# Optimization experiments

Measured on AMD Instinct MI355X. Metric: run time of the kernel, lower is better.

## Reference

```python
import jax, jax.numpy as jnp
import numpy as np

T_STEPS, N, STATE, HID, ACT, C = 32, 64, 64, 128, 32, 96


def setup_inputs() -> dict:
    key = jax.random.key(0)
    ks = jax.random.split(key, 16)
    s = 0.05
    inp = {
        'x': jax.random.normal(ks[0], (T_STEPS, N, STATE), jnp.float32),
        'a': jax.random.normal(ks[1], (T_STEPS, N, ACT), jnp.float32),
        # GRU layer 0 (input state_dim) and layer 1 (input hidden_dim)
        'wih0': jax.random.normal(ks[2], (3 * HID, STATE), jnp.float32) * s,
        'whh0': jax.random.normal(ks[3], (3 * HID, HID), jnp.float32) * s,
        'bih0': jax.random.normal(ks[4], (3 * HID,), jnp.float32) * s,
        'bhh0': jax.random.normal(ks[5], (3 * HID,), jnp.float32) * s,
        'wih1': jax.random.normal(ks[6], (3 * HID, HID), jnp.float32) * s,
        'whh1': jax.random.normal(ks[7], (3 * HID, HID), jnp.float32) * s,
        'bih1': jax.random.normal(ks[8], (3 * HID,), jnp.float32) * s,
        'bhh1': jax.random.normal(ks[9], (3 * HID,), jnp.float32) * s,
        'w1': jax.random.normal(ks[10], (HID, HID + ACT), jnp.float32) * s,
        'b1': jax.random.normal(ks[11], (HID,), jnp.float32) * s,
        'w2': jax.random.normal(ks[12], (1, 2 * HID), jnp.float32) * s,
        'b2': jax.random.normal(ks[13], (1,), jnp.float32) * s,
        'Tm': jax.random.normal(ks[14], (HID, HID, C), jnp.float32),  # init.normal(T,0,1)
    }
    return inp


def _gru_cell(x_t, h, wih, whh, bih, bhh):
    gi = x_t @ wih.T + bih            # (N, 3H)
    gh = h @ whh.T + bhh
    i_r, i_z, i_n = jnp.split(gi, 3, axis=-1)
    h_r, h_z, h_n = jnp.split(gh, 3, axis=-1)
    r = jax.nn.sigmoid(i_r + h_r)
    z = jax.nn.sigmoid(i_z + h_z)
    n = jnp.tanh(i_n + r * h_n)
    return (1.0 - z) * n + z * h


def reference(x, a, wih0, whh0, bih0, bhh0, wih1, whh1, bih1, bhh1, w1, b1, w2, b2, Tm):
    def step(h, x_t):
        h0 = _gru_cell(x_t, h[0], wih0, whh0, bih0, bhh0)
        h1 = _gru_cell(h0, h[1], wih1, whh1, bih1, bhh1)
        return jnp.stack([h0, h1]), h1

    h_init = jnp.zeros((2, N, HID), x.dtype)
    _, p = jax.lax.scan(step, h_init, x)              # (T, N, H)

    fc1 = jax.nn.relu(jnp.concatenate([p, a], -1) @ w1.T + b1)  # (T, N, H)

    Tflat = Tm.reshape(HID, HID * C)

    def batch_discrim(xt):  # xt: (N, H)
        M = (xt @ Tflat).reshape(N, HID, C)           # (N, B, C)
        # pairwise L1 over C: (N, N, B)
        norm = jnp.abs(M[:, None] - M[None, :]).sum(-1)
        o_b = (jnp.exp(-norm).sum(0) - 1.0) / (N - 1)  # (N, B)
        return jnp.concatenate([xt, o_b], 1)          # (N, 2H)

    fc2 = jax.lax.map(batch_discrim, fc1)             # (T, N, 2H)
    prob = jax.nn.sigmoid(fc2 @ w2.T + b2)            # (T, N, 1)
    return prob
```

## Files before the change

### kernel.cpp

```cpp
#include <hip/hip_runtime.h>
#include <hip/hip_fp16.h>
#include <cstdint>

#define T_STEPS 32
#define NB 64
#define STATE 64
#define HID 128
#define ACT 32
#define CDIM 96
#define G3 (3*HID)

typedef __attribute__((ext_vector_type(8))) short short8;
typedef __attribute__((ext_vector_type(4))) float f32x4;
typedef _Float16 h2v __attribute__((ext_vector_type(2)));

__device__ __forceinline__ unsigned short f2bf(float f){
  unsigned int u = __builtin_bit_cast(unsigned int, f);
  u = u + 0x7FFFu + ((u >> 16) & 1u);
  return (unsigned short)(u >> 16);
}
__device__ __forceinline__ float bf2f(unsigned short u){
  unsigned int v = ((unsigned int)u) << 16; return __builtin_bit_cast(float, v);
}
__device__ __forceinline__ unsigned int packh2(float f0, float f1){
  return (unsigned int)__half_as_ushort(__float2half_rn(f0)) |
         ((unsigned int)__half_as_ushort(__float2half_rn(f1)) << 16);
}
__device__ __forceinline__ float sigmoidf_(float x){ return 1.0f/(1.0f + __expf(-x)); }
__device__ __forceinline__ float tanhf_(float x){ float e = __expf(2.0f*x); return (e-1.0f)/(e+1.0f); }

__device__ __forceinline__ float dot2f(float acc, unsigned int a, unsigned int b){
  h2v av = __builtin_bit_cast(h2v, a);
  h2v bv = __builtin_bit_cast(h2v, b);
  return __builtin_amdgcn_fdot2(av, bv, acc, false);
}
__device__ __forceinline__ float l1d(float acc, unsigned int ua, unsigned int ub){
  __half2 a = __builtin_bit_cast(__half2, ua);
  __half2 b = __builtin_bit_cast(__half2, ub);
  __half2 d = __habs2(__hsub2(a, b));
  h2v dv = __builtin_bit_cast(h2v, d);
  h2v ones; ones[0] = (_Float16)1.0f; ones[1] = (_Float16)1.0f;
  return __builtin_amdgcn_fdot2(dv, ones, acc, false);
}
__device__ __forceinline__ float l1d4(float acc, uint4 a, uint4 b){
  acc = l1d(acc, a.x, b.x); acc = l1d(acc, a.y, b.y);
  acc = l1d(acc, a.z, b.z); acc = l1d(acc, a.w, b.w);
  return acc;
}

__global__ void k_prep(const float* __restrict__ Tm, unsigned short* __restrict__ tmh,
                       const float* __restrict__ whh0, const float* __restrict__ whh1,
                       const float* __restrict__ w1, const float* __restrict__ wih0,
                       const float* __restrict__ wih1, const float* __restrict__ x,
                       const float* __restrict__ a,
                       unsigned int* __restrict__ whh0p, unsigned int* __restrict__ whh1p,
                       unsigned short* __restrict__ w1f, unsigned short* __restrict__ wi0f,
                       unsigned short* __restrict__ wi1f, unsigned short* __restrict__ xaf,
                       unsigned short* __restrict__ h1af){
  __shared__ __align__(4) unsigned short lt[12800];
  int tid = threadIdx.x;
  int bx = blockIdx.x;
  if (bx < 128){
    int b = bx;
    unsigned int* l2 = (unsigned int*)lt;
    for (int e4 = tid; e4 < 3072; e4 += 256){
      int k = e4 / 24, c4 = (e4 - k*24)*4;
      const float4 v = *(const float4*)(Tm + k*(HID*CDIM) + b*CDIM + c4);
      int base = (k*100 + c4) >> 1;
      l2[base]   = (unsigned int)f2bf(v.x) | ((unsigned int)f2bf(v.y) << 16);
      l2[base+1] = (unsigned int)f2bf(v.z) | ((unsigned int)f2bf(v.w) << 16);
    }
    __syncthreads();
    unsigned int* tm2 = (unsigned int*)(tmh + b*(HID*CDIM));
    for (int e2 = tid; e2 < 6144; e2 += 256){
      int e = e2*2;
      int chunk = e / 768;
      int r1 = e - chunk*768;
      int c = r1 >> 3, h = r1 & 7;
      unsigned int lo = lt[(chunk*8 + h)*100 + c];
      unsigned int hi = lt[(chunk*8 + h + 1)*100 + c];
      tm2[e2] = lo | (hi << 16);
    }
  } else if (bx < 132){
    for (int e = (bx-128)*256 + tid; e < 24576; e += 1024){
      int k2 = e / 384, r = e - k2*384;
      whh0p[e] = packh2(whh0[r*128 + 2*k2], whh0[r*128 + 2*k2 + 1]);
      whh1p[e] = packh2(whh1[r*128 + 2*k2], whh1[r*128 + 2*k2 + 1]);
    }
  } else if (bx < 136){
    for (int e = (bx-132)*256 + tid; e < 20480; e += 1024){
      int kc = e >> 10, rem = e & 1023;
      int col = rem >> 3, j = rem & 7;
      w1f[e] = f2bf(w1[col*160 + kc*8 + j]);
    }
  } else if (bx < 140){
    for (int e = (bx-136)*256 + tid; e < 24576; e += 1024){
      int kc = e / 3072, rem = e - kc*3072;
      int col = rem >> 3, kl = rem & 7;
      wi0f[e] = f2bf(wih0[col*64 + kc*8 + kl]);
    }
  } else if (bx < 144){
    for (int e = (bx-140)*256 + tid; e < 49152; e += 1024){
      int kc = e / 3072, rem = e - kc*3072;
      int col = rem >> 3, kl = rem & 7;
      wi1f[e] = f2bf(wih1[col*128 + kc*8 + kl]);
    }
  } else if (bx < 156){
    for (int e = (bx-144)*256 + tid; e < 131072; e += 3072){
      int t = e >> 12, rem = e & 4095;
      int ntile = rem >> 10, rem2 = rem & 1023;
      int kc = rem2 >> 7, nl = (rem2 >> 3) & 15, kl = rem2 & 7;
      int n = ntile*16 + nl, k = kc*8 + kl;
      xaf[e] = f2bf(x[t*4096 + n*64 + k]);
    }
  } else {
    for (int e = (bx-156)*256 + tid; e < 65536; e += 3072){
      int t = e >> 11, rem = e & 2047;
      int n = rem >> 5, c = rem & 31;
      int pos = t*10240 + (n>>4)*2560 + (16 + (c>>3))*128 + (n&15)*8 + (c&7);
      h1af[pos] = f2bf(a[t*(NB*ACT) + n*ACT + c]);
    }
  }
}

template<int KK, int TSU>
__global__ __launch_bounds__(256) void k_gi(const unsigned short* __restrict__ af,
                                            const unsigned short* __restrict__ wf,
                                            const float* __restrict__ bias,
                                            float* __restrict__ gig){
  int t = blockIdx.x, by = blockIdx.y, tid = threadIdx.x;
  int wave = tid >> 6, lane = tid & 63, m = lane & 15, quad = lane >> 4;
  const uint4* A4 = (const uint4*)af;
  const uint4* B4 = (const uint4*)wf;
  uint4 av[KK];
  #pragma unroll
  for (int kk = 0; kk < KK; kk++) av[kk] = A4[t*TSU + wave*(TSU/4) + (kk*4+quad)*16 + m];
  f32x4 acc[6];
  #pragma unroll
  for (int i = 0; i < 6; i++) acc[i] = (f32x4)(0.0f);
  #pragma unroll
  for (int kk = 0; kk < KK; kk++){
    short8 a = __builtin_bit_cast(short8, av[kk]);
    #pragma unroll
    for (int ntl = 0; ntl < 6; ntl++){
      int nt = by*6 + ntl;
      uint4 bv = B4[(kk*4+quad)*384 + nt*16 + m];
      acc[ntl] = __builtin_amdgcn_mfma_f32_16x16x32_bf16(a, __builtin_bit_cast(short8, bv), acc[ntl], 0, 0, 0);
    }
  }
  #pragma unroll
  for (int ntl = 0; ntl < 6; ntl++){
    int col = (by*6+ntl)*16 + m;
    float bv = bias[col];
    #pragma unroll
    for (int rr = 0; rr < 4; rr++){
      int n = wave*16 + quad*4 + rr;
      gig[(t*NB + n)*G3 + col] = acc[ntl][rr] + bv;
    }
  }
}

template<int TS, int NS>
__global__ __launch_bounds__(768, 3) void k_rec(const unsigned int* __restrict__ whhp,
                                                const float* __restrict__ bhh,
                                                const float* __restrict__ gig,
                                                unsigned short* __restrict__ haf){
  __shared__ __align__(16) unsigned int hl[64];
  __shared__ float A0[G3];
  int n = blockIdx.x, tid = threadIdx.x;
  int r = tid >> 1, kh = tid & 1;
  unsigned int wh[32];
  #pragma unroll
  for (int i = 0; i < 32; i++) wh[i] = whhp[(kh*32 + i)*384 + r];
  float bh = (kh == 0) ? bhh[r] : 0.0f;
  if (tid < 64) hl[tid] = 0u;
  float g_r = 0.0f, g_z = 0.0f, g_n = 0.0f, hprev = 0.0f;
  if (tid < HID){
    const float* gp = gig + n*G3 + tid;
    g_r = gp[0]; g_z = gp[HID]; g_n = gp[2*HID];
  }
  __syncthreads();
  const uint4* h4 = (const uint4*)hl;
  for (int t = 0; t < T_STEPS; t++){
    float s0 = 0.0f, s1 = 0.0f, s2 = 0.0f, s3 = 0.0f;
    #pragma unroll
    for (int g = 0; g < 2; g++){
      uint4 hv[4];
      #pragma unroll
      for (int j = 0; j < 4; j++) hv[j] = h4[kh*8 + g*4 + j];
      s0 = dot2f(s0, wh[g*16 + 0], hv[0].x);  s0 = dot2f(s0, wh[g*16 + 1], hv[0].y);
      s0 = dot2f(s0, wh[g*16 + 2], hv[0].z);  s0 = dot2f(s0, wh[g*16 + 3], hv[0].w);
      s1 = dot2f(s1, wh[g*16 + 4], hv[1].x);  s1 = dot2f(s1, wh[g*16 + 5], hv[1].y);
      s1 = dot2f(s1, wh[g*16 + 6], hv[1].z);  s1 = dot2f(s1, wh[g*16 + 7], hv[1].w);
      s2 = dot2f(s2, wh[g*16 + 8], hv[2].x);  s2 = dot2f(s2, wh[g*16 + 9], hv[2].y);
      s2 = dot2f(s2, wh[g*16 +10], hv[2].z);  s2 = dot2f(s2, wh[g*16 +11], hv[2].w);
      s3 = dot2f(s3, wh[g*16 +12], hv[3].x);  s3 = dot2f(s3, wh[g*16 +13], hv[3].y);
      s3 = dot2f(s3, wh[g*16 +14], hv[3].z);  s3 = dot2f(s3, wh[g*16 +15], hv[3].w);
    }
    float gh = bh + ((s0 + s1) + (s2 + s3));
    gh += __shfl_xor(gh, 1);
    if (kh == 0) A0[r] = gh;
    __syncthreads();
    if (tid < HID){
      float cr = g_r, cz = g_z, cn = g_n;
      int tn2 = (t+1 < T_STEPS) ? t+1 : t;
      const float* gp = gig + (tn2*NB + n)*G3 + tid;
      g_r = gp[0]; g_z = gp[HID]; g_n = gp[2*HID];
      float rg = sigmoidf_(cr + A0[tid]);
      float z  = sigmoidf_(cz + A0[tid+HID]);
      float nn = tanhf_   (cn + rg*A0[tid+2*HID]);
      float hn = (1.0f - z)*nn + z*hprev;
      hprev = hn;
      ((__half*)hl)[tid] = __float2half_rn(hn);
      haf[t*TS + (n>>4)*NS + (tid>>3)*128 + (n&15)*8 + (tid&7)] = f2bf(hn);
    }
    __syncthreads();
  }
}

__global__ __launch_bounds__(256) void k_fc1(const unsigned short* __restrict__ h1af,
                                             const unsigned short* __restrict__ w1f,
                                             const float* __restrict__ b1,
                                             unsigned short* __restrict__ fc1h){
  __shared__ float b1s[128];
  int t = blockIdx.x, tid = threadIdx.x;
  int wave = tid >> 6, lane = tid & 63, m = lane & 15, quad = lane >> 4;
  if (tid < 128) b1s[tid] = b1[tid];
  const uint4* A4 = (const uint4*)(h1af + t*10240);
  const uint4* B4 = (const uint4*)w1f;
  f32x4 acc[8];
  #pragma unroll
  for (int i = 0; i < 8; i++) acc[i] = (f32x4)(0.0f);
  #pragma unroll
  for (int ks = 0; ks < 5; ks++){
    uint4 av = A4[wave*320 + (ks*4 + quad)*16 + m];
    short8 avs = __builtin_bit_cast(short8, av);
    #pragma unroll
    for (int nt = 0; nt < 8; nt++){
      uint4 bv = B4[(ks*4 + quad)*128 + nt*16 + m];
      acc[nt] = __builtin_amdgcn_mfma_f32_16x16x32_bf16(avs, __builtin_bit_cast(short8, bv), acc[nt], 0, 0, 0);
    }
  }
  __syncthreads();
  #pragma unroll
  for (int nt = 0; nt < 8; nt++){
    float bj = b1s[nt*16 + m];
    #pragma unroll
    for (int rr = 0; rr < 4; rr++){
      float v = fmaxf(acc[nt][rr] + bj, 0.0f);
      fc1h[t*8192 + wave*2048 + (nt*2 + (m>>3))*128 + (quad*4 + rr)*8 + (m&7)] = f2bf(v);
    }
  }
}

__global__ __launch_bounds__(256) void k_disc(const unsigned short* __restrict__ fc1h,
                                              const unsigned short* __restrict__ tmh,
                                              float* __restrict__ O){
  __shared__ __align__(16) __half Mh[64*120];
  __shared__ unsigned short plist[2016];
  __shared__ float osum[64];
  __shared__ unsigned int cnt;
  int b = blockIdx.x, t = blockIdx.y;
  int tid = threadIdx.x;
  int wave = tid >> 6, lane = tid & 63, m = lane & 15, quad = lane >> 4;
  if (tid < 64) osum[tid] = 0.0f;
  if (tid == 0) cnt = 0u;
  const uint4* Bg = (const uint4*)(tmh + b*(CDIM*HID));
  const uint4* Ag = (const uint4*)(fc1h + t*8192);
  uint4 a4[4];
  #pragma unroll
  for (int kk = 0; kk < 4; kk++) a4[kk] = Ag[wave*256 + (kk*4 + quad)*16 + m];
  f32x4 acc[6];
  #pragma unroll
  for (int i = 0; i < 6; i++) acc[i] = (f32x4)(0.0f);
  #pragma unroll
  for (int kk = 0; kk < 4; kk++){
    short8 av = __builtin_bit_cast(short8, a4[kk]);
    #pragma unroll
    for (int nt = 0; nt < 6; nt++){
      uint4 b4 = Bg[(kk*4 + quad)*96 + nt*16 + m];
      acc[nt] = __builtin_amdgcn_mfma_f32_16x16x32_bf16(av, __builtin_bit_cast(short8, b4), acc[nt], 0, 0, 0);
    }
  }
  #pragma unroll
  for (int nt = 0; nt < 6; nt++){
    #pragma unroll
    for (int rr = 0; rr < 4; rr++){
      Mh[(wave*16 + quad*4 + rr)*120 + nt*16 + m] = __float2half(acc[nt][rr]);
    }
  }
  __syncthreads();
  const unsigned int ONES2 = 0x3C003C00u;
  #pragma unroll
  for (int idx = tid; idx < 512; idx += 256){
    int r = idx >> 3, jc = idx & 7;
    const unsigned int* row = (const unsigned int*)(Mh + r*120 + jc*12);
    float s = 0.0f;
    #pragma unroll
    for (int q = 0; q < 6; q++) s = dot2f(s, row[q], ONES2);
    Mh[r*120 + 96 + jc] = __float2half(s);
  }
  __syncthreads();
  const uint4* M4 = (const uint4*)Mh;
  for (int p = tid; p < 2016; p += 256){
    int r = p >> 5, s = p & 31;
    int i, j;
    if (s == 0){ i = 63; j = r; }
    else {
      i = r + s;      if (i >= 63) i -= 63;
      j = r + 63 - s; if (j >= 63) j -= 63;
    }
    uint4 qa = M4[i*15 + 12];
    uint4 qb = M4[j*15 + 12];
    float lb = l1d4(0.0f, qa, qb);
    if (lb <= 14.5f){
      unsigned int k = atomicAdd(&cnt, 1u);
      plist[k] = (unsigned short)(i*64 + j);
    }
  }
  __syncthreads();
  int ns = (int)cnt;
  if (ns > 2016) ns = 2016;
  for (int v = tid; v < ns; v += 256){
    int pr = plist[v];
    int i = pr >> 6, j = pr & 63;
    float L = 0.0f;
    #pragma unroll
    for (int c = 0; c < 12; c++){
      L = l1d4(L, M4[i*15 + c], M4[j*15 + c]);
    }
    float e = __expf(-L);
    atomicAdd(&osum[i], e);
    atomicAdd(&osum[j], e);
  }
  __syncthreads();
  if (tid < 64) O[(t*HID + b)*NB + tid] = osum[tid]*(1.0f/63.0f);
}

__global__ __launch_bounds__(256) void k_final(const unsigned short* __restrict__ fc1h,
                                               const float* __restrict__ O,
                                               const float* __restrict__ w2, const float* __restrict__ b2,
                                               float* __restrict__ out){
  __shared__ float ol[NB*HID];
  __shared__ unsigned short fr[8192];
  __shared__ float wl[2*HID + 2];
  __shared__ float pp[4][NB];
  int t = blockIdx.x, tid = threadIdx.x;
  for (int i = tid; i < NB*HID; i += 256) ol[i] = O[t*NB*HID + i];
  const uint4* Fg = (const uint4*)(fc1h + t*8192);
  for (int i = tid; i < 1024; i += 256) ((uint4*)fr)[i] = Fg[i];
  if (tid < 2*HID) wl[tid] = w2[tid];
  if (tid == 0) wl[2*HID] = b2[0];
  __syncthreads();
  int n = tid & 63, part = tid >> 6;
  float acc = 0.0f;
  int base = (n>>4)*2048 + (n&15)*8;
  #pragma unroll
  for (int jc = 0; jc < 4; jc++){
    int j8 = part*4 + jc;
    #pragma unroll
    for (int k = 0; k < 8; k++)
      acc += bf2f(fr[base + j8*128 + k])*wl[j8*8 + k];
  }
  #pragma unroll 8
  for (int bb = 0; bb < 32; bb++){
    int bq = part*32 + bb;
    acc += ol[bq*NB + n]*wl[HID + bq];
  }
  pp[part][n] = acc;
  __syncthreads();
  if (tid < NB){
    float s = wl[2*HID] + pp[0][tid] + pp[1][tid] + pp[2][tid] + pp[3][tid];
    out[t*NB + tid] = sigmoidf_(s);
  }
}

extern "C" void kernel_launch(void* const* d_in, const int* in_sizes, int n_in,
                              void* d_out, int out_size, void* d_ws, size_t ws_size,
                              hipStream_t stream){
  const float* x    = (const float*)d_in[0];
  const float* a    = (const float*)d_in[1];
  const float* wih0 = (const float*)d_in[2];
  const float* whh0 = (const float*)d_in[3];
  const float* bih0 = (const float*)d_in[4];
  const float* bhh0 = (const float*)d_in[5];
  const float* wih1 = (const float*)d_in[6];
  const float* whh1 = (const float*)d_in[7];
  const float* bih1 = (const float*)d_in[8];
  const float* bhh1 = (const float*)d_in[9];
  const float* w1   = (const float*)d_in[10];
  const float* b1   = (const float*)d_in[11];
  const float* w2   = (const float*)d_in[12];
  const float* b2   = (const float*)d_in[13];
  const float* Tm   = (const float*)d_in[14];
  float* ws = (float*)d_ws;
  float* Ows = ws;
  unsigned int* whh0p = (unsigned int*)(ws + 262144);
  unsigned int* whh1p = (unsigned int*)(ws + 286720);
  unsigned short* tmh  = (unsigned short*)(ws + 311296);
  unsigned short* fc1h = (unsigned short*)(ws + 1097728);
  unsigned short* h1af = (unsigned short*)(ws + 1228800);
  unsigned short* w1f  = (unsigned short*)(ws + 1392640);
  unsigned short* xaf  = (unsigned short*)(ws + 1402880);
  unsigned short* wi0f = (unsigned short*)(ws + 1468416);
  unsigned short* wi1f = (unsigned short*)(ws + 1480704);
  unsigned short* h0af = (unsigned short*)(ws + 1505280);
  float* gig = ws + 1636352;
  float* out = (float*)d_out;

  k_prep<<<dim3(168), dim3(256), 0, stream>>>(Tm, tmh, whh0, whh1, w1, wih0, wih1, x, a,
                                              whh0p, whh1p, w1f, wi0f, wi1f, xaf, h1af);
  k_gi<2, 512><<<dim3(T_STEPS, 4), dim3(256), 0, stream>>>(xaf, wi0f, bih0, gig);
  k_rec<8192, 2048><<<dim3(NB), dim3(768), 0, stream>>>(whh0p, bhh0, gig, h0af);
  k_gi<4, 1024><<<dim3(T_STEPS, 4), dim3(256), 0, stream>>>(h0af, wi1f, bih1, gig);
  k_rec<10240, 2560><<<dim3(NB), dim3(768), 0, stream>>>(whh1p, bhh1, gig, h1af);
  k_fc1<<<dim3(T_STEPS), dim3(256), 0, stream>>>(h1af, w1f, b1, fc1h);
  k_disc<<<dim3(HID, T_STEPS), dim3(256), 0, stream>>>(fc1h, tmh, Ows);
  k_final<<<dim3(T_STEPS), dim3(256), 0, stream>>>(fc1h, Ows, w2, b2, out);
}
```

Measured before the change: 189.9 us.

## Fuse layer-1 input projection into layer-0 recurrence kernel

The layer-1 input-gate projection (h0 @ wih1.T + bih1) is now computed inside the layer-0 recurrent kernel. It uses fp16 dot2 against register-resident packed weights, reusing the h0 vector already in LDS, and writes gates one step late. This removes the separate k_gi launch for layer 1 and the bf16 h0 staging buffer. It also replaces __syncthreads with an explicit lgkmcnt wait plus s_barrier. In exchange, the serial recurrence does extra per-step work and holds more registers, and the input projection moves from bf16 MFMA to fp16 dot2 precision.

After: 210.9 us. 1.11x slower.

```diff
diff --git a/kernel.cpp b/kernel.cpp
--- a/kernel.cpp
+++ b/kernel.cpp
@@ -48,15 +48,22 @@
   return acc;
 }
 
+__device__ __forceinline__ void barrier_lds(){
+  __builtin_amdgcn_sched_barrier(0);
+  asm volatile("s_waitcnt lgkmcnt(0)" ::: "memory");
+  __builtin_amdgcn_s_barrier();
+  __builtin_amdgcn_sched_barrier(0);
+}
+
 __global__ void k_prep(const float* __restrict__ Tm, unsigned short* __restrict__ tmh,
                        const float* __restrict__ whh0, const float* __restrict__ whh1,
                        const float* __restrict__ w1, const float* __restrict__ wih0,
                        const float* __restrict__ wih1, const float* __restrict__ x,
                        const float* __restrict__ a,
                        unsigned int* __restrict__ whh0p, unsigned int* __restrict__ whh1p,
+                       unsigned int* __restrict__ wi1p,
                        unsigned short* __restrict__ w1f, unsigned short* __restrict__ wi0f,
-                       unsigned short* __restrict__ wi1f, unsigned short* __restrict__ xaf,
-                       unsigned short* __restrict__ h1af){
+                       unsigned short* __restrict__ xaf, unsigned short* __restrict__ h1af){
   __shared__ __align__(4) unsigned short lt[12800];
   int tid = threadIdx.x;
   int bx = blockIdx.x;
@@ -86,6 +93,7 @@
       int k2 = e / 384, r = e - k2*384;
       whh0p[e] = packh2(whh0[r*128 + 2*k2], whh0[r*128 + 2*k2 + 1]);
       whh1p[e] = packh2(whh1[r*128 + 2*k2], whh1[r*128 + 2*k2 + 1]);
+      wi1p[e]  = packh2(wih1[r*128 + 2*k2], wih1[r*128 + 2*k2 + 1]);
     }
   } else if (bx < 136){
     for (int e = (bx-132)*256 + tid; e < 20480; e += 1024){
@@ -99,14 +107,8 @@
       int col = rem >> 3, kl = rem & 7;
       wi0f[e] = f2bf(wih0[col*64 + kc*8 + kl]);
     }
-  } else if (bx < 144){
-    for (int e = (bx-140)*256 + tid; e < 49152; e += 1024){
-      int kc = e / 3072, rem = e - kc*3072;
-      int col = rem >> 3, kl = rem & 7;
-      wi1f[e] = f2bf(wih1[col*128 + kc*8 + kl]);
-    }
-  } else if (bx < 156){
-    for (int e = (bx-144)*256 + tid; e < 131072; e += 3072){
+  } else if (bx < 152){
+    for (int e = (bx-140)*256 + tid; e < 131072; e += 3072){
       int t = e >> 12, rem = e & 4095;
       int ntile = rem >> 10, rem2 = rem & 1023;
       int kc = rem2 >> 7, nl = (rem2 >> 3) & 15, kl = rem2 & 7;
@@ -114,7 +116,7 @@
       xaf[e] = f2bf(x[t*4096 + n*64 + k]);
     }
   } else {
-    for (int e = (bx-156)*256 + tid; e < 65536; e += 3072){
+    for (int e = (bx-152)*256 + tid; e < 65536; e += 3072){
       int t = e >> 11, rem = e & 2047;
       int n = rem >> 5, c = rem & 31;
       int pos = t*10240 + (n>>4)*2560 + (16 + (c>>3))*128 + (n&15)*8 + (c&7);
@@ -160,11 +162,14 @@
   }
 }
 
-template<int TS, int NS>
+template<int TS, int NS, bool GI1>
 __global__ __launch_bounds__(768, 3) void k_rec(const unsigned int* __restrict__ whhp,
                                                 const float* __restrict__ bhh,
                                                 const float* __restrict__ gig,
-                                                unsigned short* __restrict__ haf){
+                                                unsigned short* __restrict__ haf,
+                                                const unsigned int* __restrict__ wip,
+                                                const float* __restrict__ bi1,
+                                                float* __restrict__ gog){
   __shared__ __align__(16) unsigned int hl[64];
   __shared__ float A0[G3];
   int n = blockIdx.x, tid = threadIdx.x;
@@ -173,6 +178,13 @@
   #pragma unroll
   for (int i = 0; i < 32; i++) wh[i] = whhp[(kh*32 + i)*384 + r];
   float bh = (kh == 0) ? bhh[r] : 0.0f;
+  unsigned int wi[GI1 ? 32 : 1];
+  float bi = 0.0f;
+  if constexpr (GI1){
+    #pragma unroll
+    for (int i = 0; i < 32; i++) wi[i] = wip[(kh*32 + i)*384 + r];
+    bi = (kh == 0) ? bi1[r] : 0.0f;
+  }
   if (tid < 64) hl[tid] = 0u;
   float g_r = 0.0f, g_z = 0.0f, g_n = 0.0f, hprev = 0.0f;
   if (tid < HID){
@@ -183,6 +195,7 @@
   const uint4* h4 = (const uint4*)hl;
   for (int t = 0; t < T_STEPS; t++){
     float s0 = 0.0f, s1 = 0.0f, s2 = 0.0f, s3 = 0.0f;
+    float q0 = 0.0f, q1 = 0.0f, q2 = 0.0f, q3 = 0.0f;
     #pragma unroll
     for (int g = 0; g < 2; g++){
       uint4 hv[4];
@@ -196,11 +209,26 @@
       s2 = dot2f(s2, wh[g*16 +10], hv[2].z);  s2 = dot2f(s2, wh[g*16 +11], hv[2].w);
       s3 = dot2f(s3, wh[g*16 +12], hv[3].x);  s3 = dot2f(s3, wh[g*16 +13], hv[3].y);
       s3 = dot2f(s3, wh[g*16 +14], hv[3].z);  s3 = dot2f(s3, wh[g*16 +15], hv[3].w);
+      if constexpr (GI1){
+        q0 = dot2f(q0, wi[g*16 + 0], hv[0].x);  q0 = dot2f(q0, wi[g*16 + 1], hv[0].y);
+        q0 = dot2f(q0, wi[g*16 + 2], hv[0].z);  q0 = dot2f(q0, wi[g*16 + 3], hv[0].w);
+        q1 = dot2f(q1, wi[g*16 + 4], hv[1].x);  q1 = dot2f(q1, wi[g*16 + 5], hv[1].y);
+        q1 = dot2f(q1, wi[g*16 + 6], hv[1].z);  q1 = dot2f(q1, wi[g*16 + 7], hv[1].w);
+        q2 = dot2f(q2, wi[g*16 + 8], hv[2].x);  q2 = dot2f(q2, wi[g*16 + 9], hv[2].y);
+        q2 = dot2f(q2, wi[g*16 +10], hv[2].z);  q2 = dot2f(q2, wi[g*16 +11], hv[2].w);
+        q3 = dot2f(q3, wi[g*16 +12], hv[3].x);  q3 = dot2f(q3, wi[g*16 +13], hv[3].y);
+        q3 = dot2f(q3, wi[g*16 +14], hv[3].z);  q3 = dot2f(q3, wi[g*16 +15], hv[3].w);
+      }
     }
     float gh = bh + ((s0 + s1) + (s2 + s3));
     gh += __shfl_xor(gh, 1);
     if (kh == 0) A0[r] = gh;
-    __syncthreads();
+    if constexpr (GI1){
+      float gi = bi + ((q0 + q1) + (q2 + q3));
+      gi += __shfl_xor(gi, 1);
+      if (kh == 0 && t > 0) gog[((t-1)*NB + n)*G3 + r] = gi;
+    }
+    barrier_lds();
     if (tid < HID){
       float cr = g_r, cz = g_z, cn = g_n;
       int tn2 = (t+1 < T_STEPS) ? t+1 : t;
@@ -212,9 +240,30 @@
       float hn = (1.0f - z)*nn + z*hprev;
       hprev = hn;
       ((__half*)hl)[tid] = __float2half_rn(hn);
-      haf[t*TS + (n>>4)*NS + (tid>>3)*128 + (n&15)*8 + (tid&7)] = f2bf(hn);
-    }
-    __syncthreads();
+      if constexpr (!GI1)
+        haf[t*TS + (n>>4)*NS + (tid>>3)*128 + (n&15)*8 + (tid&7)] = f2bf(hn);
+    }
+    barrier_lds();
+  }
+  if constexpr (GI1){
+    float q0 = 0.0f, q1 = 0.0f, q2 = 0.0f, q3 = 0.0f;
+    #pragma unroll
+    for (int g = 0; g < 2; g++){
+      uint4 hv[4];
+      #pragma unroll
+      for (int j = 0; j < 4; j++) hv[j] = h4[kh*8 + g*4 + j];
+      q0 = dot2f(q0, wi[g*16 + 0], hv[0].x);  q0 = dot2f(q0, wi[g*16 + 1], hv[0].y);
+      q0 = dot2f(q0, wi[g*16 + 2], hv[0].z);  q0 = dot2f(q0, wi[g*16 + 3], hv[0].w);
+      q1 = dot2f(q1, wi[g*16 + 4], hv[1].x);  q1 = dot2f(q1, wi[g*16 + 5], hv[1].y);
+      q1 = dot2f(q1, wi[g*16 + 6], hv[1].z);  q1 = dot2f(q1, wi[g*16 + 7], hv[1].w);
+      q2 = dot2f(q2, wi[g*16 + 8], hv[2].x);  q2 = dot2f(q2, wi[g*16 + 9], hv[2].y);
+      q2 = dot2f(q2, wi[g*16 +10], hv[2].z);  q2 = dot2f(q2, wi[g*16 +11], hv[2].w);
+      q3 = dot2f(q3, wi[g*16 +12], hv[3].x);  q3 = dot2f(q3, wi[g*16 +13], hv[3].y);
+      q3 = dot2f(q3, wi[g*16 +14], hv[3].z);  q3 = dot2f(q3, wi[g*16 +15], hv[3].w);
+    }
+    float gi = bi + ((q0 + q1) + (q2 + q3));
+    gi += __shfl_xor(gi, 1);
+    if (kh == 0) gog[((T_STEPS-1)*NB + n)*G3 + r] = gi;
   }
 }
 
@@ -403,17 +452,18 @@
   unsigned short* w1f  = (unsigned short*)(ws + 1392640);
   unsigned short* xaf  = (unsigned short*)(ws + 1402880);
   unsigned short* wi0f = (unsigned short*)(ws + 1468416);
-  unsigned short* wi1f = (unsigned short*)(ws + 1480704);
-  unsigned short* h0af = (unsigned short*)(ws + 1505280);
-  float* gig = ws + 1636352;
+  unsigned int*   wi1p = (unsigned int*)(ws + 1480704);
+  float* gig  = ws + 1636352;
+  float* gig1 = ws + 2422784;
   float* out = (float*)d_out;
 
-  k_prep<<<dim3(168), dim3(256), 0, stream>>>(Tm, tmh, whh0, whh1, w1, wih0, wih1, x, a,
-                                              whh0p, whh1p, w1f, wi0f, wi1f, xaf, h1af);
+  k_prep<<<dim3(164), dim3(256), 0, stream>>>(Tm, tmh, whh0, whh1, w1, wih0, wih1, x, a,
+                                              whh0p, whh1p, wi1p, w1f, wi0f, xaf, h1af);
   k_gi<2, 512><<<dim3(T_STEPS, 4), dim3(256), 0, stream>>>(xaf, wi0f, bih0, gig);
-  k_rec<8192, 2048><<<dim3(NB), dim3(768), 0, stream>>>(whh0p, bhh0, gig, h0af);
-  k_gi<4, 1024><<<dim3(T_STEPS, 4), dim3(256), 0, stream>>>(h0af, wi1f, bih1, gig);
-  k_rec<10240, 2560><<<dim3(NB), dim3(768), 0, stream>>>(whh1p, bhh1, gig, h1af);
+  k_rec<8192, 2048, true><<<dim3(NB), dim3(768), 0, stream>>>(whh0p, bhh0, gig, nullptr,
+                                                              wi1p, bih1, gig1);
+  k_rec<10240, 2560, false><<<dim3(NB), dim3(768), 0, stream>>>(whh1p, bhh1, gig1, h1af,
+                                                                nullptr, nullptr, nullptr);
   k_fc1<<<dim3(T_STEPS), dim3(256), 0, stream>>>(h1af, w1f, b1, fc1h);
   k_disc<<<dim3(HID, T_STEPS), dim3(256), 0, stream>>>(fc1h, tmh, Ows);
   k_final<<<dim3(T_STEPS), dim3(256), 0, stream>>>(fc1h, Ows, w2, b2, out);
```

## Stage recurrent gate inputs and hidden history in LDS, bulk-write outputs

Applied to the files above, without the earlier changes.

The recurrent GRU kernel now preloads all timesteps of its precomputed input gates into shared memory with vectorized float4 loads before the loop. Previously it prefetched one step ahead from global memory inside the serial loop. Hidden outputs are buffered in a shared history array and written out at the end as 16-byte stores, replacing scattered 2-byte global stores each step. This takes global latency off the serial critical path, at the cost of about 57KB of extra LDS per block, which may lower occupancy.

Result: faster. 184.4 us (-2.9%).

```diff
diff --git a/kernel.cpp b/kernel.cpp
--- a/kernel.cpp
+++ b/kernel.cpp
@@ -167,18 +167,26 @@
                                                 unsigned short* __restrict__ haf){
   __shared__ __align__(16) unsigned int hl[64];
   __shared__ float A0[G3];
+  __shared__ __align__(16) float gl[T_STEPS*G3];
+  __shared__ __align__(16) unsigned short hist[T_STEPS*HID];
   int n = blockIdx.x, tid = threadIdx.x;
   int r = tid >> 1, kh = tid & 1;
+  {
+    const float4* gg = (const float4*)gig;
+    float4* gl4 = (float4*)gl;
+    #pragma unroll
+    for (int k = 0; k < 4; k++){
+      int e = k*768 + tid;
+      int t = e / 96, c = e - t*96;
+      gl4[t*96 + c] = gg[(t*NB + n)*96 + c];
+    }
+  }
   unsigned int wh[32];
   #pragma unroll
   for (int i = 0; i < 32; i++) wh[i] = whhp[(kh*32 + i)*384 + r];
   float bh = (kh == 0) ? bhh[r] : 0.0f;
   if (tid < 64) hl[tid] = 0u;
-  float g_r = 0.0f, g_z = 0.0f, g_n = 0.0f, hprev = 0.0f;
-  if (tid < HID){
-    const float* gp = gig + n*G3 + tid;
-    g_r = gp[0]; g_z = gp[HID]; g_n = gp[2*HID];
-  }
+  float hprev = 0.0f;
   __syncthreads();
   const uint4* h4 = (const uint4*)hl;
   for (int t = 0; t < T_STEPS; t++){
@@ -202,19 +210,21 @@
     if (kh == 0) A0[r] = gh;
     __syncthreads();
     if (tid < HID){
-      float cr = g_r, cz = g_z, cn = g_n;
-      int tn2 = (t+1 < T_STEPS) ? t+1 : t;
-      const float* gp = gig + (tn2*NB + n)*G3 + tid;
-      g_r = gp[0]; g_z = gp[HID]; g_n = gp[2*HID];
-      float rg = sigmoidf_(cr + A0[tid]);
-      float z  = sigmoidf_(cz + A0[tid+HID]);
-      float nn = tanhf_   (cn + rg*A0[tid+2*HID]);
+      const float* gp = gl + t*G3;
+      float rg = sigmoidf_(gp[tid]       + A0[tid]);
+      float z  = sigmoidf_(gp[tid+HID]   + A0[tid+HID]);
+      float nn = tanhf_   (gp[tid+2*HID] + rg*A0[tid+2*HID]);
       float hn = (1.0f - z)*nn + z*hprev;
       hprev = hn;
       ((__half*)hl)[tid] = __float2half_rn(hn);
-      haf[t*TS + (n>>4)*NS + (tid>>3)*128 + (n&15)*8 + (tid&7)] = f2bf(hn);
+      hist[t*HID + tid] = f2bf(hn);
     }
     __syncthreads();
+  }
+  if (tid < T_STEPS*16){
+    int t = tid >> 4, j = tid & 15;
+    uint4 v = *(const uint4*)(hist + t*HID + j*8);
+    *(uint4*)(haf + t*TS + (n>>4)*NS + j*128 + (n&15)*8) = v;
   }
 }
 
```
